# Optimization experiments

Hardware: AMD Instinct MI355X
Metric: run time of the kernel (lower is better)

## Reference

```python
import jax, jax.numpy as jnp
import numpy as np

B, M, N, C = 8192, 16, 256, 64


def setup_inputs() -> dict:
    key = jax.random.key(0)
    k1, k2 = jax.random.split(key)
    inputs = jax.random.normal(k1, (B, M, C), dtype=jnp.float32)
    codebook = jax.random.normal(k2, (M, N, C), dtype=jnp.float32)
    return {"inputs": inputs, "codebook": codebook}


def reference(inputs, codebook):
    # inputs: [B, M, C]; codebook: [M, N, C]
    # (avoids materializing the torch [B, M, N, C] broadcast difference)
    x2 = jnp.sum(inputs * inputs, axis=-1)[:, :, None]          # [B, M, 1]
    c2 = jnp.sum(codebook * codebook, axis=-1)[None, :, :]      # [1, M, N]
    xc = jnp.einsum('bmc,mnc->bmn', inputs, codebook)           # [B, M, N]
    dist = x2 - 2.0 * xc + c2                                   # [B, M, N]
    idx = jnp.argmin(dist, axis=-1)                             # [B, M] int
    m_idx = jnp.arange(codebook.shape[0])[None, :]              # [1, M]
    codes = codebook[m_idx, idx]                                # [B, M, C]
    return codes, idx
```

## Files before the change

### kernel.cpp

```cpp
#include <hip/hip_runtime.h>
#include <hip/hip_bf16.h>
#include <float.h>


#define BQ 8192
#define MQ 16
#define NQ 256
#define CQ 64
#define RPB 512

typedef short  shortx8 __attribute__((ext_vector_type(8)));
typedef float  f32x4   __attribute__((ext_vector_type(4)));

#define HI_MASK 0xffff0000u

__device__ __forceinline__ void split3_pair(float a, float b,
                                            uint& q0, uint& q1, uint& q2) {
    const uint ba = __builtin_bit_cast(uint, a);
    const uint bb = __builtin_bit_cast(uint, b);
    q0 = (ba >> 16) | (bb & HI_MASK);
    const float r1a = a - __builtin_bit_cast(float, ba & HI_MASK);
    const float r1b = b - __builtin_bit_cast(float, bb & HI_MASK);
    const uint c1a = __builtin_bit_cast(uint, r1a);
    const uint c1b = __builtin_bit_cast(uint, r1b);
    q1 = (c1a >> 16) | (c1b & HI_MASK);
    const float r2a = r1a - __builtin_bit_cast(float, c1a & HI_MASK);
    const float r2b = r1b - __builtin_bit_cast(float, c1b & HI_MASK);
    q2 = (__builtin_bit_cast(uint, r2a) >> 16) |
         (__builtin_bit_cast(uint, r2b) & HI_MASK);
}

__global__ __launch_bounds__(512, 2) void fq_fused_kernel(
        const float* __restrict__ inputs,
        const float* __restrict__ codebook,
        float* __restrict__ out_codes,
        float* __restrict__ out_idx) {
    const int m    = blockIdx.y;
    const int rowB = blockIdx.x * RPB;
    const int w    = (int)threadIdx.x >> 6;
    const int lane = (int)threadIdx.x & 63;
    const int quad = lane >> 4;
    const int col  = lane & 15;

    __shared__ unsigned short lds_b[96 * 512];
    __shared__ float s_c2v[NQ];

    const float* cbm = codebook + (size_t)m * NQ * CQ;
    #pragma unroll
    for (int it = 0; it < 4; ++it) {
        const int item = (int)threadIdx.x + it * 512;
        const int kc = item & 7;
        const int n  = item >> 3;
        const int nt = n >> 4, cc = n & 15;
        const int h = kc >> 2, q = kc & 3;
        const float* src = cbm + (size_t)n * CQ + kc * 8;
        const float4 va = *(const float4*)src;
        const float4 vb = *(const float4*)(src + 4);
        const float el[8] = {va.x, va.y, va.z, va.w, vb.x, vb.y, vb.z, vb.w};

        float s = 0.0f;
        #pragma unroll
        for (int u = 0; u < 8; ++u) s = fmaf(el[u], el[u], s);
        s += __shfl_xor(s, 1, 64);
        s += __shfl_xor(s, 2, 64);
        s += __shfl_xor(s, 4, 64);
        if (kc == 0) s_c2v[n] = s;

        uint p0[4], p1[4], p2[4];
        #pragma unroll
        for (int u = 0; u < 4; ++u)
            split3_pair(el[2 * u], el[2 * u + 1], p0[u], p1[u], p2[u]);
        const int lf = q * 16 + cc;
        #pragma unroll
        for (int j = 0; j < 3; ++j) {
            const uint* p = (j == 0) ? p0 : (j == 1) ? p1 : p2;
            unsigned short* dst =
                &lds_b[(((j << 1) + h) * 16 + nt) * 512 + lf * 8];
            *(uint4*)dst = make_uint4(p[0], p[1], p[2], p[3]);
        }
    }
    __syncthreads();

    #pragma unroll 1
    for (int tt = 0; tt < 2; ++tt) {
        const int row0 = rowB + w * 64 + tt * 32;

        shortx8 afr[3][2][2];
        #pragma unroll
        for (int rt = 0; rt < 2; ++rt) {
            const float* xb =
                inputs + ((size_t)(row0 + rt * 16 + col) * MQ + m) * CQ;
            #pragma unroll
            for (int h = 0; h < 2; ++h) {
                const float4 va = *(const float4*)(xb + h * 32 + quad * 8);
                const float4 vb = *(const float4*)(xb + h * 32 + quad * 8 + 4);
                const float el[8] = {va.x, va.y, va.z, va.w,
                                     vb.x, vb.y, vb.z, vb.w};
                uint q0[4], q1[4], q2[4];
                #pragma unroll
                for (int u = 0; u < 4; ++u)
                    split3_pair(el[2 * u], el[2 * u + 1], q0[u], q1[u], q2[u]);
                afr[0][rt][h] = __builtin_bit_cast(shortx8,
                    make_uint4(q0[0], q0[1], q0[2], q0[3]));
                afr[1][rt][h] = __builtin_bit_cast(shortx8,
                    make_uint4(q1[0], q1[1], q1[2], q1[3]));
                afr[2][rt][h] = __builtin_bit_cast(shortx8,
                    make_uint4(q2[0], q2[1], q2[2], q2[3]));
            }
        }

        float bd0[2][4]; int bi0[2][4];
        #pragma unroll 1
        for (int chh = 0; chh < 2; ++chh) {
            float c2r[8];
            #pragma unroll
            for (int nt = 0; nt < 8; ++nt)
                c2r[nt] = s_c2v[chh * 128 + nt * 16 + col];

            f32x4 acc[2][8];
            #pragma unroll
            for (int rt = 0; rt < 2; ++rt)
                #pragma unroll
                for (int nt = 0; nt < 8; ++nt)
                    acc[rt][nt] = (f32x4){0.f, 0.f, 0.f, 0.f};

            #pragma unroll
            for (int h = 0; h < 2; ++h) {
                #pragma unroll
                for (int j = 0; j < 3; ++j) {
                    shortx8 bfr[8];
                    #pragma unroll
                    for (int nt = 0; nt < 8; ++nt)
                        bfr[nt] = *(const shortx8*)
                            &lds_b[(((j << 1) + h) * 16 + chh * 8 + nt) * 512
                                   + lane * 8];
                    #pragma unroll
                    for (int i = 0; i <= 2 - j; ++i) {
                        #pragma unroll
                        for (int nt = 0; nt < 8; ++nt) {
                            acc[0][nt] = __builtin_amdgcn_mfma_f32_16x16x32_bf16(
                                afr[i][0][h], bfr[nt], acc[0][nt], 0, 0, 0);
                            acc[1][nt] = __builtin_amdgcn_mfma_f32_16x16x32_bf16(
                                afr[i][1][h], bfr[nt], acc[1][nt], 0, 0, 0);
                        }
                    }
                }
            }

            #pragma unroll
            for (int rt = 0; rt < 2; ++rt) {
                #pragma unroll
                for (int reg = 0; reg < 4; ++reg) {
                    float bd = FLT_MAX; int bi = 0;
                    #pragma unroll
                    for (int nt = 0; nt < 8; ++nt) {
                        const float d = fmaf(-2.0f, acc[rt][nt][reg], c2r[nt]);
                        if (d < bd) { bd = d; bi = chh * 128 + nt * 16 + col; }
                    }
                    #pragma unroll
                    for (int mask = 1; mask <= 8; mask <<= 1) {
                        const float od = __shfl_xor(bd, mask, 64);
                        const int   oi = __shfl_xor(bi, mask, 64);
                        if (od < bd || (od == bd && oi < bi)) { bd = od; bi = oi; }
                    }
                    if (chh == 0) { bd0[rt][reg] = bd; bi0[rt][reg] = bi; }
                    else {
                        if (bd < bd0[rt][reg] ||
                            (bd == bd0[rt][reg] && bi < bi0[rt][reg])) {
                            bd0[rt][reg] = bd; bi0[rt][reg] = bi;
                        }
                    }
                }
            }
        }

        if (col == 0) {
            #pragma unroll
            for (int rt = 0; rt < 2; ++rt)
                #pragma unroll
                for (int reg = 0; reg < 4; ++reg)
                    out_idx[(size_t)(row0 + rt * 16 + quad * 4 + reg) * MQ + m] =
                        (float)bi0[rt][reg];
        }

        #pragma unroll
        for (int jj = 0; jj < 32; ++jj) {
            const int rt  = jj >> 4;
            const int r16 = jj & 15;
            const int bn  = __shfl(bi0[rt][r16 & 3], (r16 >> 2) * 16, 64);
            out_codes[((size_t)(row0 + jj) * MQ + m) * CQ + lane] =
                cbm[(size_t)bn * CQ + lane];
        }
    }
}

extern "C" void kernel_launch(void* const* d_in, const int* in_sizes, int n_in,
                              void* d_out, int out_size, void* d_ws, size_t ws_size,
                              hipStream_t stream) {
    const float* inputs   = (const float*)d_in[0];
    const float* codebook = (const float*)d_in[1];
    float* out_codes = (float*)d_out;
    float* out_idx   = (float*)d_out + (size_t)BQ * MQ * CQ;
    (void)d_ws; (void)ws_size;

    fq_fused_kernel<<<dim3(BQ / RPB, MQ), 512, 0, stream>>>(
        inputs, codebook, out_codes, out_idx);
}
```

Before: 113.7 us.

## Use 1024-thread blocks with one row tile per wave and per-lane argmin

Each block now runs 1024 threads (16 waves), so each wave handles a single 32-row tile instead of looping over two. The N dimension is processed in four chunks of 64 with smaller accumulator arrays, which cuts register pressure. Argmin candidates are kept per lane across chunks and reduced across lanes by shuffle only once at the end. MFMA sections are wrapped in s_setprio to raise wave priority. The aim is more resident waves for latency hiding and fewer cross-lane reductions, at the cost of more barrier participants and a tighter register budget under launch_bounds(1024,4).

```diff
diff --git a/kernel.cpp b/kernel.cpp
--- a/kernel.cpp
+++ b/kernel.cpp
@@ -30,7 +30,7 @@
          (__builtin_bit_cast(uint, r2b) & HI_MASK);
 }
 
-__global__ __launch_bounds__(512, 2) void fq_fused_kernel(
+__global__ __launch_bounds__(1024, 4) void fq_fused_kernel(
         const float* __restrict__ inputs,
         const float* __restrict__ codebook,
         float* __restrict__ out_codes,
@@ -47,8 +47,8 @@
 
     const float* cbm = codebook + (size_t)m * NQ * CQ;
     #pragma unroll
-    for (int it = 0; it < 4; ++it) {
-        const int item = (int)threadIdx.x + it * 512;
+    for (int it = 0; it < 2; ++it) {
+        const int item = (int)threadIdx.x + it * 1024;
         const int kc = item & 7;
         const int n  = item >> 3;
         const int nt = n >> 4, cc = n & 15;
@@ -81,116 +81,121 @@
     }
     __syncthreads();
 
+    const int row0 = rowB + w * 32;
+
+    shortx8 afr[3][2][2];
+    #pragma unroll
+    for (int rt = 0; rt < 2; ++rt) {
+        const float* xb =
+            inputs + ((size_t)(row0 + rt * 16 + col) * MQ + m) * CQ;
+        #pragma unroll
+        for (int h = 0; h < 2; ++h) {
+            const float4 va = *(const float4*)(xb + h * 32 + quad * 8);
+            const float4 vb = *(const float4*)(xb + h * 32 + quad * 8 + 4);
+            const float el[8] = {va.x, va.y, va.z, va.w,
+                                 vb.x, vb.y, vb.z, vb.w};
+            uint q0[4], q1[4], q2[4];
+            #pragma unroll
+            for (int u = 0; u < 4; ++u)
+                split3_pair(el[2 * u], el[2 * u + 1], q0[u], q1[u], q2[u]);
+            afr[0][rt][h] = __builtin_bit_cast(shortx8,
+                make_uint4(q0[0], q0[1], q0[2], q0[3]));
+            afr[1][rt][h] = __builtin_bit_cast(shortx8,
+                make_uint4(q1[0], q1[1], q1[2], q1[3]));
+            afr[2][rt][h] = __builtin_bit_cast(shortx8,
+                make_uint4(q2[0], q2[1], q2[2], q2[3]));
+        }
+    }
+
+    float bdc[2][4]; int bic[2][4];
+    #pragma unroll
+    for (int rt = 0; rt < 2; ++rt)
+        #pragma unroll
+        for (int reg = 0; reg < 4; ++reg) { bdc[rt][reg] = FLT_MAX; bic[rt][reg] = 0; }
+
     #pragma unroll 1
-    for (int tt = 0; tt < 2; ++tt) {
-        const int row0 = rowB + w * 64 + tt * 32;
-
-        shortx8 afr[3][2][2];
-        #pragma unroll
-        for (int rt = 0; rt < 2; ++rt) {
-            const float* xb =
-                inputs + ((size_t)(row0 + rt * 16 + col) * MQ + m) * CQ;
-            #pragma unroll
-            for (int h = 0; h < 2; ++h) {
-                const float4 va = *(const float4*)(xb + h * 32 + quad * 8);
-                const float4 vb = *(const float4*)(xb + h * 32 + quad * 8 + 4);
-                const float el[8] = {va.x, va.y, va.z, va.w,
-                                     vb.x, vb.y, vb.z, vb.w};
-                uint q0[4], q1[4], q2[4];
+    for (int cq = 0; cq < 4; ++cq) {
+        float c2r[4];
+        #pragma unroll
+        for (int nt = 0; nt < 4; ++nt)
+            c2r[nt] = s_c2v[cq * 64 + nt * 16 + col];
+
+        f32x4 acc[2][4];
+        #pragma unroll
+        for (int rt = 0; rt < 2; ++rt)
+            #pragma unroll
+            for (int nt = 0; nt < 4; ++nt)
+                acc[rt][nt] = (f32x4){0.f, 0.f, 0.f, 0.f};
+
+        #pragma unroll
+        for (int h = 0; h < 2; ++h) {
+            #pragma unroll
+            for (int j = 0; j < 3; ++j) {
+                shortx8 bfr[4];
                 #pragma unroll
-                for (int u = 0; u < 4; ++u)
-                    split3_pair(el[2 * u], el[2 * u + 1], q0[u], q1[u], q2[u]);
-                afr[0][rt][h] = __builtin_bit_cast(shortx8,
-                    make_uint4(q0[0], q0[1], q0[2], q0[3]));
-                afr[1][rt][h] = __builtin_bit_cast(shortx8,
-                    make_uint4(q1[0], q1[1], q1[2], q1[3]));
-                afr[2][rt][h] = __builtin_bit_cast(shortx8,
-                    make_uint4(q2[0], q2[1], q2[2], q2[3]));
-            }
-        }
-
-        float bd0[2][4]; int bi0[2][4];
-        #pragma unroll 1
-        for (int chh = 0; chh < 2; ++chh) {
-            float c2r[8];
-            #pragma unroll
-            for (int nt = 0; nt < 8; ++nt)
-                c2r[nt] = s_c2v[chh * 128 + nt * 16 + col];
-
-            f32x4 acc[2][8];
-            #pragma unroll
-            for (int rt = 0; rt < 2; ++rt)
+                for (int nt = 0; nt < 4; ++nt)
+                    bfr[nt] = *(const shortx8*)
+                        &lds_b[(((j << 1) + h) * 16 + cq * 4 + nt) * 512
+                               + lane * 8];
+                __builtin_amdgcn_s_setprio(1);
                 #pragma unroll
-                for (int nt = 0; nt < 8; ++nt)
-                    acc[rt][nt] = (f32x4){0.f, 0.f, 0.f, 0.f};
-
-            #pragma unroll
-            for (int h = 0; h < 2; ++h) {
-                #pragma unroll
-                for (int j = 0; j < 3; ++j) {
-                    shortx8 bfr[8];
+                for (int i = 0; i <= 2 - j; ++i) {
                     #pragma unroll
-                    for (int nt = 0; nt < 8; ++nt)
-                        bfr[nt] = *(const shortx8*)
-                            &lds_b[(((j << 1) + h) * 16 + chh * 8 + nt) * 512
-                                   + lane * 8];
-                    #pragma unroll
-                    for (int i = 0; i <= 2 - j; ++i) {
-                        #pragma unroll
-                        for (int nt = 0; nt < 8; ++nt) {
-                            acc[0][nt] = __builtin_amdgcn_mfma_f32_16x16x32_bf16(
-                                afr[i][0][h], bfr[nt], acc[0][nt], 0, 0, 0);
-                            acc[1][nt] = __builtin_amdgcn_mfma_f32_16x16x32_bf16(
-                                afr[i][1][h], bfr[nt], acc[1][nt], 0, 0, 0);
-                        }
+                    for (int nt = 0; nt < 4; ++nt) {
+                        acc[0][nt] = __builtin_amdgcn_mfma_f32_16x16x32_bf16(
+                            afr[i][0][h], bfr[nt], acc[0][nt], 0, 0, 0);
+                        acc[1][nt] = __builtin_amdgcn_mfma_f32_16x16x32_bf16(
+                            afr[i][1][h], bfr[nt], acc[1][nt], 0, 0, 0);
                     }
                 }
+                __builtin_amdgcn_s_setprio(0);
             }
-
-            #pragma unroll
-            for (int rt = 0; rt < 2; ++rt) {
+        }
+
+        #pragma unroll
+        for (int rt = 0; rt < 2; ++rt)
+            #pragma unroll
+            for (int reg = 0; reg < 4; ++reg)
                 #pragma unroll
-                for (int reg = 0; reg < 4; ++reg) {
-                    float bd = FLT_MAX; int bi = 0;
-                    #pragma unroll
-                    for (int nt = 0; nt < 8; ++nt) {
-                        const float d = fmaf(-2.0f, acc[rt][nt][reg], c2r[nt]);
-                        if (d < bd) { bd = d; bi = chh * 128 + nt * 16 + col; }
-                    }
-                    #pragma unroll
-                    for (int mask = 1; mask <= 8; mask <<= 1) {
-                        const float od = __shfl_xor(bd, mask, 64);
-                        const int   oi = __shfl_xor(bi, mask, 64);
-                        if (od < bd || (od == bd && oi < bi)) { bd = od; bi = oi; }
-                    }
-                    if (chh == 0) { bd0[rt][reg] = bd; bi0[rt][reg] = bi; }
-                    else {
-                        if (bd < bd0[rt][reg] ||
-                            (bd == bd0[rt][reg] && bi < bi0[rt][reg])) {
-                            bd0[rt][reg] = bd; bi0[rt][reg] = bi;
-                        }
+                for (int nt = 0; nt < 4; ++nt) {
+                    const float d = fmaf(-2.0f, acc[rt][nt][reg], c2r[nt]);
+                    if (d < bdc[rt][reg]) {
+                        bdc[rt][reg] = d;
+                        bic[rt][reg] = cq * 64 + nt * 16 + col;
                     }
                 }
+    }
+
+    #pragma unroll
+    for (int rt = 0; rt < 2; ++rt)
+        #pragma unroll
+        for (int reg = 0; reg < 4; ++reg) {
+            float bd = bdc[rt][reg]; int bi = bic[rt][reg];
+            #pragma unroll
+            for (int mask = 1; mask <= 8; mask <<= 1) {
+                const float od = __shfl_xor(bd, mask, 64);
+                const int   oi = __shfl_xor(bi, mask, 64);
+                if (od < bd || (od == bd && oi < bi)) { bd = od; bi = oi; }
             }
-        }
-
-        if (col == 0) {
-            #pragma unroll
-            for (int rt = 0; rt < 2; ++rt)
-                #pragma unroll
-                for (int reg = 0; reg < 4; ++reg)
-                    out_idx[(size_t)(row0 + rt * 16 + quad * 4 + reg) * MQ + m] =
-                        (float)bi0[rt][reg];
-        }
-
-        #pragma unroll
-        for (int jj = 0; jj < 32; ++jj) {
-            const int rt  = jj >> 4;
-            const int r16 = jj & 15;
-            const int bn  = __shfl(bi0[rt][r16 & 3], (r16 >> 2) * 16, 64);
-            out_codes[((size_t)(row0 + jj) * MQ + m) * CQ + lane] =
-                cbm[(size_t)bn * CQ + lane];
-        }
+            bdc[rt][reg] = bd; bic[rt][reg] = bi;
+        }
+
+    if (col == 0) {
+        #pragma unroll
+        for (int rt = 0; rt < 2; ++rt)
+            #pragma unroll
+            for (int reg = 0; reg < 4; ++reg)
+                out_idx[(size_t)(row0 + rt * 16 + quad * 4 + reg) * MQ + m] =
+                    (float)bic[rt][reg];
+    }
+
+    #pragma unroll
+    for (int jj = 0; jj < 32; ++jj) {
+        const int rt  = jj >> 4;
+        const int r16 = jj & 15;
+        const int bn  = __shfl(bic[rt][r16 & 3], (r16 >> 2) * 16, 64);
+        out_codes[((size_t)(row0 + jj) * MQ + m) * CQ + lane] =
+            cbm[(size_t)bn * CQ + lane];
     }
 }
 
@@ -203,6 +208,6 @@
     float* out_idx   = (float*)d_out + (size_t)BQ * MQ * CQ;
     (void)d_ws; (void)ws_size;
 
-    fq_fused_kernel<<<dim3(BQ / RPB, MQ), 512, 0, stream>>>(
+    fq_fused_kernel<<<dim3(BQ / RPB, MQ), 1024, 0, stream>>>(
         inputs, codebook, out_codes, out_idx);
 }
```

Result: faster. 105.0 us (-7.7%).
